# Optimization experiments

Hardware: AMD Instinct MI355X
Metric: run time of the kernel (lower is better)

## Reference

```python
import jax, jax.numpy as jnp
import numpy as np

B, S, D_IN, D_OUT, H = 4, 2048, 1024, 1024, 16
D_HEAD = D_OUT // H


def setup_inputs() -> dict:
    key = jax.random.key(0)
    ks = jax.random.split(key, 6)
    sc = 0.02
    return {
        "x": jax.random.normal(ks[0], (B, S, D_IN), dtype=jnp.float32),
        "Wq": jax.random.normal(ks[1], (D_IN, D_OUT), dtype=jnp.float32) * sc,
        "Wk": jax.random.normal(ks[2], (D_IN, D_OUT), dtype=jnp.float32) * sc,
        "Wv": jax.random.normal(ks[3], (D_IN, D_OUT), dtype=jnp.float32) * sc,
        "Wo": jax.random.normal(ks[4], (D_OUT, D_OUT), dtype=jnp.float32) * sc,
        "bo": jnp.zeros((D_OUT,), dtype=jnp.float32),
    }


def reference(x, Wq, Wk, Wv, Wo, bo):
    n_batch, n_tok, _ = x.shape
    # QKV projections (no bias), reshape to [B, H, S, Dh]
    q = (x @ Wq).reshape(n_batch, n_tok, H, D_HEAD).transpose(0, 2, 1, 3)
    k = (x @ Wk).reshape(n_batch, n_tok, H, D_HEAD).transpose(0, 2, 1, 3)
    v = (x @ Wv).reshape(n_batch, n_tok, H, D_HEAD).transpose(0, 2, 1, 3)
    # scores [B, H, S, S], causal mask, scaled softmax
    scores = jnp.einsum('bhqd,bhkd->bhqk', q, k)
    causal = jnp.tril(jnp.ones((n_tok, n_tok), dtype=bool))
    scores = jnp.where(causal, scores, -jnp.inf)
    attn = jax.nn.softmax(scores / jnp.sqrt(jnp.float32(D_HEAD)), axis=-1)
    # dropout in eval mode -> identity
    ctx = jnp.einsum('bhqk,bhkd->bhqd', attn, v)
    ctx = ctx.transpose(0, 2, 1, 3).reshape(n_batch, n_tok, D_OUT)
    return ctx @ Wo + bo
```

## Files before the change

### kernel.cpp

```cpp
#include <hip/hip_runtime.h>


#define S_LEN 2048
#define DMODEL 1024
#define NB 4

typedef unsigned short u16;
typedef unsigned int u32;
typedef float f32x4 __attribute__((ext_vector_type(4)));
typedef float f32x16 __attribute__((ext_vector_type(16)));
typedef int i32x4 __attribute__((ext_vector_type(4)));
typedef short s16x8 __attribute__((ext_vector_type(8)));
typedef __bf16 bf16x8 __attribute__((ext_vector_type(8)));

__device__ __forceinline__ u16 f2bf(float f) {
  return __builtin_bit_cast(u16, (__bf16)f);
}

__device__ __forceinline__ f32x4 mfma16(s16x8 a, s16x8 b, f32x4 c) {
  return __builtin_amdgcn_mfma_f32_16x16x32_bf16(
      __builtin_bit_cast(bf16x8, a), __builtin_bit_cast(bf16x8, b), c, 0, 0, 0);
}

__device__ __forceinline__ f32x16 mfma32(s16x8 a, s16x8 b, f32x16 c) {
  return __builtin_amdgcn_mfma_f32_32x32x16_bf16(
      __builtin_bit_cast(bf16x8, a), __builtin_bit_cast(bf16x8, b), c, 0, 0, 0);
}

__device__ __forceinline__ int cvtpk(float a, float b) {
  int r;
  asm("v_cvt_pk_bf16_f32 %0, %1, %2" : "=v"(r) : "v"(a), "v"(b));
  return r;
}

__device__ __forceinline__ void gload_lds16(void* lds, const void* g) {
  __builtin_amdgcn_global_load_lds(
      (const __attribute__((address_space(1))) void*)g,
      (__attribute__((address_space(3))) void*)lds, 16, 0, 0);
}

__device__ __forceinline__ s16x8 lds_frag(const u16* lds, int row, int colb) {
  int addr = (row << 7) + (colb ^ ((row & 7) << 4));
  return *(const s16x8*)((const char*)lds + addr);
}

struct G8 {
  u16 As[3][256 * 64];
  u16 Bs[3][128 * 64];
};

template <int NT>
__device__ __forceinline__ void gemm8ph(const u16* __restrict__ A,
                                        const u16* __restrict__ Bt,
                                        int m0, int n0, G8& L,
                                        f32x4 (&acc)[4][4], int tid) {
  constexpr int K = NT * 64;
  const int lane = tid & 63;
  const int wr = (tid >> 6) >> 1, wc = (tid >> 6) & 1;

  auto SA = [&](int buf, int kt) {
    const u16* g = A + (size_t)m0 * K + kt * 64;
    #pragma unroll
    for (int it = 0; it < 4; ++it) {
      int o = (tid + it * 512) << 4;
      int r = o >> 7, c = o & 127;
      gload_lds16((char*)L.As[buf] + o,
                  (const char*)(g + (size_t)r * K) + (c ^ ((r & 7) << 4)));
    }
  };
  auto SB = [&](int buf, int kt) {
    const u16* g = Bt + (size_t)n0 * K + kt * 64;
    #pragma unroll
    for (int it = 0; it < 2; ++it) {
      int o = (tid + it * 512) << 4;
      int r = o >> 7, c = o & 127;
      gload_lds16((char*)L.Bs[buf] + o,
                  (const char*)(g + (size_t)r * K) + (c ^ ((r & 7) << 4)));
    }
  };

  SA(0, 0); SB(0, 0);
  SA(1, 1); SB(1, 1);
  asm volatile("s_waitcnt vmcnt(6)" ::: "memory");
  asm volatile("s_barrier" ::: "memory");

  int cb = 0;
  for (int t = 0; t < NT; ++t) {
    const u16* Ac = L.As[cb];
    const u16* Bc = L.Bs[cb];
    int nxt = cb + 2; if (nxt >= 3) nxt -= 3;
    bool pf = (t + 2 < NT);
    #pragma unroll
    for (int ph = 0; ph < 2; ++ph) {
      s16x8 a[4], b[4];
      #pragma unroll
      for (int f = 0; f < 4; ++f) {
        a[f] = lds_frag(Ac, wr * 64 + f * 16 + (lane & 15), ph * 64 + ((lane >> 4) << 4));
        b[f] = lds_frag(Bc, wc * 64 + f * 16 + (lane & 15), ph * 64 + ((lane >> 4) << 4));
      }
      if (pf) { if (ph == 0) SA(nxt, t + 2); else SB(nxt, t + 2); }
      __builtin_amdgcn_s_setprio(1);
      #pragma unroll
      for (int mf = 0; mf < 4; ++mf)
        #pragma unroll
        for (int nf = 0; nf < 4; ++nf)
          acc[mf][nf] = mfma16(a[mf], b[nf], acc[mf][nf]);
      __builtin_amdgcn_s_setprio(0);
    }
    if (pf) asm volatile("s_waitcnt vmcnt(6)" ::: "memory");
    else    asm volatile("s_waitcnt vmcnt(0)" ::: "memory");
    asm volatile("s_barrier" ::: "memory");
    cb = (cb + 1 == 3) ? 0 : cb + 1;
  }
}

__global__ __launch_bounds__(256) void castx_kernel(const float4* __restrict__ x,
                                                    ushort4* __restrict__ xb) {
  int i = blockIdx.x * 256 + threadIdx.x;
  float4 v = x[i];
  ushort4 o;
  o.x = f2bf(v.x); o.y = f2bf(v.y); o.z = f2bf(v.z); o.w = f2bf(v.w);
  xb[i] = o;
}

__global__ __launch_bounds__(256) void wtrans_kernel(
    const float* __restrict__ W0, const float* __restrict__ W1,
    const float* __restrict__ W2, const float* __restrict__ W3,
    u16* __restrict__ T0, u16* __restrict__ T1, u16* __restrict__ T2, u16* __restrict__ T3) {
  int z = blockIdx.z;
  const float* W = (z == 0) ? W0 : (z == 1) ? W1 : (z == 2) ? W2 : W3;
  u16* T = (z == 0) ? T0 : (z == 1) ? T1 : (z == 2) ? T2 : T3;
  __shared__ float t[32][33];
  int n0 = blockIdx.x << 5, k0 = blockIdx.y << 5;
  int tx = threadIdx.x & 31, ty = threadIdx.x >> 5;
  #pragma unroll
  for (int j = 0; j < 4; ++j)
    t[ty + (j << 3)][tx] = W[(size_t)(k0 + ty + (j << 3)) * DMODEL + n0 + tx];
  __syncthreads();
  #pragma unroll
  for (int j = 0; j < 4; ++j)
    T[(size_t)(n0 + ty + (j << 3)) * DMODEL + k0 + tx] = f2bf(t[tx][ty + (j << 3)]);
}

__global__ __launch_bounds__(512, 2) void qkv8_kernel(
    const u16* __restrict__ xb, const u16* __restrict__ WqkvT,
    u16* __restrict__ Qo, u16* __restrict__ Ko, u16* __restrict__ Vto) {
  __shared__ G8 L;
  int bid = blockIdx.x;
  int f = (bid & 7) * 96 + (bid >> 3);
  int m0 = (f / 24) << 8, n0 = (f % 24) << 7;
  int tid = threadIdx.x, lane = tid & 63;
  int wr = (tid >> 6) >> 1, wc = (tid >> 6) & 1;
  f32x4 acc[4][4] = {};
  gemm8ph<16>(xb, WqkvT, m0, n0, L, acc, tid);
  int z = n0 >> 10;
  if (z == 2) {
    #pragma unroll
    for (int mf = 0; mf < 4; ++mf)
      #pragma unroll
      for (int nf = 0; nf < 4; ++nf) {
        int rm = m0 + wr * 64 + mf * 16 + ((lane >> 4) << 2);
        int cn = n0 + wc * 64 + nf * 16 + (lane & 15);
        int bb = rm >> 11, s = rm & (S_LEN - 1);
        int c1 = cn & 1023, h = c1 >> 6, d = c1 & 63;
        u32 p0 = (u32)cvtpk(acc[mf][nf][0], acc[mf][nf][1]);
        u32 p1 = (u32)cvtpk(acc[mf][nf][2], acc[mf][nf][3]);
        u32* dst = (u32*)(Vto + (((size_t)((bb << 4) + h)) << 17) + ((size_t)d << 11) + s);
        dst[0] = p0; dst[1] = p1;
      }
  } else {
    float scale = (z == 0) ? 0.18033688f : 1.0f;
    u16* out = (z == 0) ? Qo : Ko;
    #pragma unroll
    for (int mf = 0; mf < 4; ++mf)
      #pragma unroll
      for (int nf = 0; nf < 4; ++nf)
        #pragma unroll
        for (int i = 0; i < 4; ++i) {
          int rm = m0 + wr * 64 + mf * 16 + ((lane >> 4) << 2) + i;
          int cn = n0 + wc * 64 + nf * 16 + (lane & 15);
          int bb = rm >> 11, s = rm & (S_LEN - 1);
          int c1 = cn & 1023, h = c1 >> 6, d = c1 & 63;
          out[((size_t)((bb << 4) + h) << 17) + ((size_t)s << 6) + d] =
              f2bf(acc[mf][nf][i] * scale);
        }
  }
}

__global__ __launch_bounds__(256, 2) void attn_kernel(const u16* __restrict__ Q,
                                                      const u16* __restrict__ K,
                                                      const u16* __restrict__ Vt,
                                                      u16* __restrict__ ctx) {
  __shared__ u16 Ks[2][2][64 * 64];
  __shared__ u16 Vts[2][2][64 * 64];
  int bh = blockIdx.x, pid = blockIdx.y;
  int tid = threadIdx.x, lane = tid & 63, w = tid >> 6;
  int hi = lane >> 5, lq = lane & 31;
  const u16* Qb = Q + ((size_t)bh << 17);
  const u16* Kb = K + ((size_t)bh << 17);
  const u16* Vtb = Vt + ((size_t)bh << 17);
  int bb = bh >> 4, h = bh & 15;

  auto stage_pair = [&](int pb, int tp) {
    #pragma unroll
    for (int s = 0; s < 2; ++s) {
      int k0 = (tp * 2 + s) << 6;
      #pragma unroll
      for (int it = 0; it < 2; ++it) {
        int o = (tid + (it << 8)) << 4;
        int r = o >> 7, c = o & 127;
        int csrc = c ^ ((r & 7) << 4);
        gload_lds16((char*)Ks[pb][s] + o,
                    (const char*)(Kb + ((size_t)(k0 + r) << 6)) + csrc);
        gload_lds16((char*)Vts[pb][s] + o,
                    (const char*)(Vtb + ((size_t)r << 11) + k0) + csrc);
      }
    }
  };

  for (int ph = 0; ph < 2; ++ph) {
    int qblk = ph ? (15 - pid) : pid;
    int q0 = qblk << 7;
    int qw = q0 + (w << 5);
    int q = qw + lq;

    s16x8 qf[4];
    #pragma unroll
    for (int t = 0; t < 4; ++t)
      qf[t] = *(const s16x8*)(Qb + ((size_t)q << 6) + t * 16 + (hi << 3));

    f32x16 acc_o[2] = {};
    float l_acc = 0.0f;

    int npairs = (q0 >> 7) + 1;
    stage_pair(0, 0);
    __syncthreads();
    for (int tp = 0; tp < npairs; ++tp) {
      int pb = tp & 1;
      if (tp + 1 < npairs) stage_pair(pb ^ 1, tp + 1);
      #pragma unroll
      for (int s = 0; s < 2; ++s) {
        int t = tp * 2 + s;
        int k0 = t << 6;
        if (k0 > qw + 31) continue;
        const u16* Kc = Ks[pb][s];
        const u16* Vc = Vts[pb][s];

        #pragma unroll
        for (int kvb = 0; kvb < 2; ++kvb) {
          int kb0 = k0 + kvb * 32;
          if (kb0 <= qw + 31) {
            f32x16 sc = {};
            #pragma unroll
            for (int tt = 0; tt < 4; ++tt) {
              s16x8 kf = lds_frag(Kc, kvb * 32 + lq, tt * 32 + (hi << 4));
              sc = mfma32(kf, qf[tt], sc);
            }
            if (kb0 + 31 > qw) {
              #pragma unroll
              for (int r = 0; r < 16; ++r) {
                int kv = kb0 + (r & 3) + ((r >> 2) << 3) + (hi << 2);
                sc[r] = (kv <= q) ? sc[r] : -3.0e38f;
              }
            }
            #pragma unroll
            for (int r = 0; r < 16; ++r) sc[r] = __builtin_amdgcn_exp2f(sc[r]);
            #pragma unroll
            for (int r = 0; r < 16; ++r) l_acc += sc[r];

            #pragma unroll
            for (int tt = 0; tt < 2; ++tt) {
              int x0 = cvtpk(sc[8 * tt + 0], sc[8 * tt + 1]);
              int x1 = cvtpk(sc[8 * tt + 2], sc[8 * tt + 3]);
              int y0 = cvtpk(sc[8 * tt + 4], sc[8 * tt + 5]);
              int y1 = cvtpk(sc[8 * tt + 6], sc[8 * tt + 7]);
              asm volatile("v_permlane32_swap_b32 %0, %1" : "+v"(x0), "+v"(y0));
              asm volatile("v_permlane32_swap_b32 %0, %1" : "+v"(x1), "+v"(y1));
              i32x4 wi = {x0, x1, y0, y1};
              s16x8 W = __builtin_bit_cast(s16x8, wi);
              int tg = kvb * 2 + tt;
              __builtin_amdgcn_s_setprio(1);
              #pragma unroll
              for (int dblk = 0; dblk < 2; ++dblk) {
                s16x8 vf = lds_frag(Vc, dblk * 32 + lq, tg * 32 + (hi << 4));
                acc_o[dblk] = mfma32(vf, W, acc_o[dblk]);
              }
              __builtin_amdgcn_s_setprio(0);
            }
          }
        }
      }
      __syncthreads();
    }

    l_acc += __shfl_xor(l_acc, 32);
    float linv = 1.0f / l_acc;
    #pragma unroll
    for (int dblk = 0; dblk < 2; ++dblk)
      #pragma unroll
      for (int rp = 0; rp < 8; ++rp) {
        int r = rp * 2;
        int pk = cvtpk(acc_o[dblk][r] * linv, acc_o[dblk][r + 1] * linv);
        int d = dblk * 32 + (r & 3) + ((r >> 2) << 3) + (hi << 2);
        *(u32*)(ctx + (((size_t)(bb << 11) + q) << 10) + (h << 6) + d) = (u32)pk;
      }
  }
}

__global__ __launch_bounds__(512, 2) void out8_kernel(const u16* __restrict__ ctx,
                                                      const u16* __restrict__ WoT,
                                                      const float* __restrict__ bo,
                                                      float* __restrict__ out) {
  __shared__ G8 L;
  int bid = blockIdx.x;
  int f = (bid & 7) * 32 + (bid >> 3);
  int m0 = (f >> 3) << 8, n0 = (f & 7) << 7;
  int tid = threadIdx.x, lane = tid & 63;
  int wr = (tid >> 6) >> 1, wc = (tid >> 6) & 1;
  f32x4 acc[4][4] = {};
  gemm8ph<16>(ctx, WoT, m0, n0, L, acc, tid);
  #pragma unroll
  for (int mf = 0; mf < 4; ++mf)
    #pragma unroll
    for (int nf = 0; nf < 4; ++nf)
      #pragma unroll
      for (int i = 0; i < 4; ++i) {
        int rm = m0 + wr * 64 + mf * 16 + ((lane >> 4) << 2) + i;
        int cn = n0 + wc * 64 + nf * 16 + (lane & 15);
        out[(size_t)rm * DMODEL + cn] = acc[mf][nf][i] + bo[cn];
      }
}

extern "C" void kernel_launch(void* const* d_in, const int* in_sizes, int n_in,
                              void* d_out, int out_size, void* d_ws, size_t ws_size,
                              hipStream_t stream) {
  const float* x  = (const float*)d_in[0];
  const float* Wq = (const float*)d_in[1];
  const float* Wk = (const float*)d_in[2];
  const float* Wv = (const float*)d_in[3];
  const float* Wo = (const float*)d_in[4];
  const float* bo = (const float*)d_in[5];
  float* out = (float*)d_out;

  char* ws = (char*)d_ws;
  const size_t SZ_T = (size_t)NB * S_LEN * DMODEL * 2;
  const size_t SZ_W = (size_t)DMODEL * DMODEL * 2;
  u16* xb  = (u16*)(ws);
  u16* WqT = (u16*)(ws + SZ_T);
  u16* WkT = (u16*)(ws + SZ_T + 1 * SZ_W);
  u16* WvT = (u16*)(ws + SZ_T + 2 * SZ_W);
  u16* WoT = (u16*)(ws + SZ_T + 3 * SZ_W);
  u16* Qb  = (u16*)(ws + 1 * SZ_T + 4 * SZ_W);
  u16* Kb  = (u16*)(ws + 2 * SZ_T + 4 * SZ_W);
  u16* Vtb = (u16*)(ws + 3 * SZ_T + 4 * SZ_W);
  u16* ctx = xb;

  castx_kernel<<<dim3((NB * S_LEN * DMODEL / 4) / 256), dim3(256), 0, stream>>>(
      (const float4*)x, (ushort4*)xb);
  wtrans_kernel<<<dim3(32, 32, 4), dim3(256), 0, stream>>>(Wq, Wk, Wv, Wo,
                                                           WqT, WkT, WvT, WoT);
  qkv8_kernel<<<dim3(768), dim3(512), 0, stream>>>(xb, WqT, Qb, Kb, Vtb);
  attn_kernel<<<dim3(64, 8), dim3(256), 0, stream>>>(Qb, Kb, Vtb, ctx);
  out8_kernel<<<dim3(256), dim3(512), 0, stream>>>(ctx, WoT, bo, out);
}
```

Before: 134.0 us.

## Rewrite QKV GEMM with 256x384 tiles and a K=32 three-stage LDS pipeline

Replaces the 256x128-tile QKV projection kernel with a dedicated kernel that uses 256x384 output tiles (one workgroup per 256-wavefront CU slot, 256 blocks) and 32-wide K slices. It uses a triple-buffered direct-to-LDS prefetch with a new 64-byte-row swizzle, and each wave holds 8x6 MFMA accumulators. The goal is to raise arithmetic intensity per LDS byte and cut the block count to exactly fill the CUs. In exchange it needs far more accumulator registers, which risks spills or lower occupancy. The smaller K step also means more barriers per unit of work.

```diff
diff --git a/kernel.cpp b/kernel.cpp
--- a/kernel.cpp
+++ b/kernel.cpp
@@ -41,6 +41,11 @@
 
 __device__ __forceinline__ s16x8 lds_frag(const u16* lds, int row, int colb) {
   int addr = (row << 7) + (colb ^ ((row & 7) << 4));
+  return *(const s16x8*)((const char*)lds + addr);
+}
+
+__device__ __forceinline__ s16x8 lds_frag32(const u16* lds, int row, int colb) {
+  int addr = (row << 6) + (colb ^ (((row >> 1) & 3) << 4));
   return *(const s16x8*)((const char*)lds + addr);
 }
 
@@ -142,49 +147,100 @@
     T[(size_t)(n0 + ty + (j << 3)) * DMODEL + k0 + tx] = f2bf(t[tx][ty + (j << 3)]);
 }
 
-__global__ __launch_bounds__(512, 2) void qkv8_kernel(
+struct G384 {
+  u16 As[3][256 * 32];
+  u16 Bs[3][384 * 32];
+};
+
+__global__ __launch_bounds__(512, 2) void qkv384_kernel(
     const u16* __restrict__ xb, const u16* __restrict__ WqkvT,
     u16* __restrict__ Qo, u16* __restrict__ Ko, u16* __restrict__ Vto) {
-  __shared__ G8 L;
+  __shared__ G384 L;
+  constexpr int K = 1024, NT = 32;
   int bid = blockIdx.x;
-  int f = (bid & 7) * 96 + (bid >> 3);
-  int m0 = (f / 24) << 8, n0 = (f % 24) << 7;
+  int m0 = (bid >> 3) << 8;
+  int n0 = (bid & 7) * 384;
   int tid = threadIdx.x, lane = tid & 63;
-  int wr = (tid >> 6) >> 1, wc = (tid >> 6) & 1;
-  f32x4 acc[4][4] = {};
-  gemm8ph<16>(xb, WqkvT, m0, n0, L, acc, tid);
-  int z = n0 >> 10;
-  if (z == 2) {
-    #pragma unroll
-    for (int mf = 0; mf < 4; ++mf)
-      #pragma unroll
-      for (int nf = 0; nf < 4; ++nf) {
-        int rm = m0 + wr * 64 + mf * 16 + ((lane >> 4) << 2);
-        int cn = n0 + wc * 64 + nf * 16 + (lane & 15);
-        int bb = rm >> 11, s = rm & (S_LEN - 1);
-        int c1 = cn & 1023, h = c1 >> 6, d = c1 & 63;
+  int wr = (tid >> 6) >> 2, wc = (tid >> 6) & 3;
+
+  auto SA = [&](int buf, int kt) {
+    const u16* g = xb + (size_t)m0 * K + kt * 32;
+    #pragma unroll
+    for (int it = 0; it < 2; ++it) {
+      int o = (tid + it * 512) << 4;
+      int r = o >> 6, c = o & 63;
+      gload_lds16((char*)L.As[buf] + o,
+                  (const char*)(g + (size_t)r * K) + (c ^ (((r >> 1) & 3) << 4)));
+    }
+  };
+  auto SB = [&](int buf, int kt) {
+    const u16* g = WqkvT + (size_t)n0 * K + kt * 32;
+    #pragma unroll
+    for (int it = 0; it < 3; ++it) {
+      int o = (tid + it * 512) << 4;
+      int r = o >> 6, c = o & 63;
+      gload_lds16((char*)L.Bs[buf] + o,
+                  (const char*)(g + (size_t)r * K) + (c ^ (((r >> 1) & 3) << 4)));
+    }
+  };
+
+  f32x4 acc[8][6] = {};
+
+  SA(0, 0); SB(0, 0);
+  SA(1, 1); SB(1, 1);
+  asm volatile("s_waitcnt vmcnt(5)" ::: "memory");
+  asm volatile("s_barrier" ::: "memory");
+
+  int cb = 0;
+  for (int t = 0; t < NT; ++t) {
+    const u16* Ac = L.As[cb];
+    const u16* Bc = L.Bs[cb];
+    int nxt = cb + 2; if (nxt >= 3) nxt -= 3;
+    bool pf = (t + 2 < NT);
+    int kcol = (lane >> 4) << 4;
+    s16x8 b[6];
+    #pragma unroll
+    for (int nf = 0; nf < 6; ++nf)
+      b[nf] = lds_frag32(Bc, wc * 96 + nf * 16 + (lane & 15), kcol);
+    if (pf) { SA(nxt, t + 2); SB(nxt, t + 2); }
+    __builtin_amdgcn_s_setprio(1);
+    #pragma unroll
+    for (int mf = 0; mf < 8; ++mf) {
+      s16x8 a = lds_frag32(Ac, wr * 128 + mf * 16 + (lane & 15), kcol);
+      #pragma unroll
+      for (int nf = 0; nf < 6; ++nf)
+        acc[mf][nf] = mfma16(a, b[nf], acc[mf][nf]);
+    }
+    __builtin_amdgcn_s_setprio(0);
+    if (pf) asm volatile("s_waitcnt vmcnt(5)" ::: "memory");
+    else    asm volatile("s_waitcnt vmcnt(0)" ::: "memory");
+    asm volatile("s_barrier" ::: "memory");
+    cb = (cb + 1 == 3) ? 0 : cb + 1;
+  }
+
+  #pragma unroll
+  for (int mf = 0; mf < 8; ++mf)
+    #pragma unroll
+    for (int nf = 0; nf < 6; ++nf) {
+      int rm = m0 + wr * 128 + mf * 16 + ((lane >> 4) << 2);
+      int cn = n0 + wc * 96 + nf * 16 + (lane & 15);
+      int z = cn >> 10, c1 = cn & 1023;
+      int bb = rm >> 11, s = rm & (S_LEN - 1);
+      int h = c1 >> 6, d = c1 & 63;
+      if (z == 2) {
         u32 p0 = (u32)cvtpk(acc[mf][nf][0], acc[mf][nf][1]);
         u32 p1 = (u32)cvtpk(acc[mf][nf][2], acc[mf][nf][3]);
         u32* dst = (u32*)(Vto + (((size_t)((bb << 4) + h)) << 17) + ((size_t)d << 11) + s);
         dst[0] = p0; dst[1] = p1;
-      }
-  } else {
-    float scale = (z == 0) ? 0.18033688f : 1.0f;
-    u16* out = (z == 0) ? Qo : Ko;
-    #pragma unroll
-    for (int mf = 0; mf < 4; ++mf)
-      #pragma unroll
-      for (int nf = 0; nf < 4; ++nf)
+      } else {
+        float scale = (z == 0) ? 0.18033688f : 1.0f;
+        u16* out = (z == 0) ? Qo : Ko;
         #pragma unroll
-        for (int i = 0; i < 4; ++i) {
-          int rm = m0 + wr * 64 + mf * 16 + ((lane >> 4) << 2) + i;
-          int cn = n0 + wc * 64 + nf * 16 + (lane & 15);
-          int bb = rm >> 11, s = rm & (S_LEN - 1);
-          int c1 = cn & 1023, h = c1 >> 6, d = c1 & 63;
-          out[((size_t)((bb << 4) + h) << 17) + ((size_t)s << 6) + d] =
+        for (int i = 0; i < 4; ++i)
+          out[((size_t)((bb << 4) + h) << 17) + ((size_t)(s + i) << 6) + d] =
               f2bf(acc[mf][nf][i] * scale);
-        }
-  }
+      }
+    }
 }
 
 __global__ __launch_bounds__(256, 2) void attn_kernel(const u16* __restrict__ Q,
@@ -359,7 +415,7 @@
       (const float4*)x, (ushort4*)xb);
   wtrans_kernel<<<dim3(32, 32, 4), dim3(256), 0, stream>>>(Wq, Wk, Wv, Wo,
                                                            WqT, WkT, WvT, WoT);
-  qkv8_kernel<<<dim3(768), dim3(512), 0, stream>>>(xb, WqT, Qb, Kb, Vtb);
+  qkv384_kernel<<<dim3(256), dim3(512), 0, stream>>>(xb, WqT, Qb, Kb, Vtb);
   attn_kernel<<<dim3(64, 8), dim3(256), 0, stream>>>(Qb, Kb, Vtb, ctx);
   out8_kernel<<<dim3(256), dim3(512), 0, stream>>>(ctx, WoT, bo, out);
 }
```

Result: slower. 136.9 us (+2.1%).
